# Optimization experiments

Measured on AMD Instinct MI355X. Metric: run time of the kernel, lower is better.

The kernel has to match this reference:

```python
import jax, jax.numpy as jnp
import numpy as np
from jax import lax

H = 64            # hidden size
NUM_LAYERS = 3
EMBED_LEN = 128
B, T = 256, 2048


def _lstm_layer(x, Wih, Whh, bih, bhh):
    """x: [B, T, in]; returns full hidden sequence [B, T, H].
    PyTorch gate order: i, f, g, o."""
    Bn = x.shape[0]
    b = bih + bhh  # [4H]
    # Precompute input contribution for all timesteps: [T, B, 4H]
    xg = jnp.einsum('bti,gi->tbg', x, Wih) + b
    h0 = jnp.zeros((Bn, H), x.dtype)
    c0 = jnp.zeros((Bn, H), x.dtype)

    def step(carry, xg_t):
        h, c = carry
        gates = xg_t + h @ Whh.T  # [B, 4H]
        i, f, g, o = jnp.split(gates, 4, axis=-1)
        i = jax.nn.sigmoid(i)
        f = jax.nn.sigmoid(f)
        g = jnp.tanh(g)
        o = jax.nn.sigmoid(o)
        c = f * c + i * g
        h = o * jnp.tanh(c)
        return (h, c), h

    (_, _), hs = lax.scan(step, (h0, c0), xg)  # hs: [T, B, H]
    return jnp.swapaxes(hs, 0, 1)              # [B, T, H]


def setup_inputs() -> dict:
    key = jax.random.key(0)
    ks = jax.random.split(key, 20)
    k = 1.0 / np.sqrt(H)  # PyTorch default init bound

    def u(kk, shape):
        return jax.random.uniform(kk, shape, jnp.float32, -k, k)

    inp = {"x": jax.random.normal(ks[0], (B, 1, T), jnp.float32)}
    in_sizes = [1, H, H]
    idx = 1
    for l in range(NUM_LAYERS):
        inp[f"Wih{l}"] = u(ks[idx], (4 * H, in_sizes[l])); idx += 1
        inp[f"Whh{l}"] = u(ks[idx], (4 * H, H)); idx += 1
        inp[f"bih{l}"] = u(ks[idx], (4 * H,)); idx += 1
        inp[f"bhh{l}"] = u(ks[idx], (4 * H,)); idx += 1
    inp["fcW"] = u(ks[idx], (EMBED_LEN, H)); idx += 1
    inp["fcb"] = u(ks[idx], (EMBED_LEN,))
    return inp


def reference(x, Wih0, Whh0, bih0, bhh0,
              Wih1, Whh1, bih1, bhh1,
              Wih2, Whh2, bih2, bhh2,
              fcW, fcb):
    # forward: transpose [B,1,T] -> [B,T,1]
    h = jnp.swapaxes(x, 1, 2)
    h = _lstm_layer(h, Wih0, Whh0, bih0, bhh0)
    h = _lstm_layer(h, Wih1, Whh1, bih1, bhh1)
    h = _lstm_layer(h, Wih2, Whh2, bih2, bhh2)
    last = h[:, -1, :]              # [B, H]
    return last @ fcW.T + fcb       # [B, EMBED_LEN]
```

## Files before the change

kernel.cpp:

```cpp
#include <hip/hip_runtime.h>

#define T_LEN 2048
#define HID 64
#define EMB 128
#define WD 8
#define NWIN (T_LEN / WD)
#define NPH (NWIN + 4)
#define PPAD (HID + 4)

typedef _Float16 half2_t __attribute__((ext_vector_type(2)));
typedef _Float16 half4 __attribute__((ext_vector_type(4)));
typedef _Float16 half8 __attribute__((ext_vector_type(8)));
typedef float f32x4 __attribute__((ext_vector_type(4)));
typedef unsigned uint4v __attribute__((ext_vector_type(4)));

#if __has_builtin(__builtin_amdgcn_exp2f)
#define EXP2F(x) __builtin_amdgcn_exp2f(x)
#else
#define EXP2F(x) exp2f(x)
#endif
#if __has_builtin(__builtin_amdgcn_rcpf)
#define RCPF(x) __builtin_amdgcn_rcpf(x)
#else
#define RCPF(x) (1.0f / (x))
#endif

#define LOG2E 1.4426950408889634f

__device__ __forceinline__ float fdot2(unsigned a, unsigned b, float c) {
    return __builtin_amdgcn_fdot2(__builtin_bit_cast(half2_t, a),
                                  __builtin_bit_cast(half2_t, b), c, false);
}

__device__ __forceinline__ float dotrow(const uint4v* w, const uint4v* g, float init) {
    float a0 = init, a1 = 0.f, a2 = 0.f, a3 = 0.f;
    #pragma unroll
    for (int q = 0; q < 8; ++q) {
        a0 = fdot2(w[q][0], g[q][0], a0);
        a1 = fdot2(w[q][1], g[q][1], a1);
        a2 = fdot2(w[q][2], g[q][2], a2);
        a3 = fdot2(w[q][3], g[q][3], a3);
    }
    return (a0 + a1) + (a2 + a3);
}

__device__ __forceinline__ uint4v pack8(float4 a, float4 b, float s) {
    half2_t h0{(_Float16)(a.x * s), (_Float16)(a.y * s)};
    half2_t h1{(_Float16)(a.z * s), (_Float16)(a.w * s)};
    half2_t h2{(_Float16)(b.x * s), (_Float16)(b.y * s)};
    half2_t h3{(_Float16)(b.z * s), (_Float16)(b.w * s)};
    uint4v q;
    q[0] = __builtin_bit_cast(unsigned, h0);
    q[1] = __builtin_bit_cast(unsigned, h1);
    q[2] = __builtin_bit_cast(unsigned, h2);
    q[3] = __builtin_bit_cast(unsigned, h3);
    return q;
}

__device__ __forceinline__ void cvt8(const float* __restrict__ Wp, float s, uint4v* dst) {
    const float4* p = reinterpret_cast<const float4*>(Wp);
    #pragma unroll
    for (int k = 0; k < 8; ++k) dst[k] = pack8(p[2 * k], p[2 * k + 1], s);
}

__global__ __launch_bounds__(512)
__attribute__((amdgpu_waves_per_eu(2, 2)))
void lstm3_fused(
    const float* __restrict__ x,
    const float* __restrict__ Wih0, const float* __restrict__ Whh0,
    const float* __restrict__ bih0, const float* __restrict__ bhh0,
    const float* __restrict__ Wih1, const float* __restrict__ Whh1,
    const float* __restrict__ bih1, const float* __restrict__ bhh1,
    const float* __restrict__ Wih2, const float* __restrict__ Whh2,
    const float* __restrict__ bih2, const float* __restrict__ bhh2,
    const float* __restrict__ fcW,  const float* __restrict__ fcb,
    float* __restrict__ out)
{
    const int b   = blockIdx.x;
    const int tid = threadIdx.x;
    const int wv  = tid >> 6;
    const int L   = tid & 63;

    __shared__ __align__(16) _Float16 h0ring[16][HID];
    __shared__ __align__(16) _Float16 h1ring[16][HID];
    __shared__ __align__(16) _Float16 h2ring[2][HID];
    __shared__ __align__(16) float p1buf[2][WD][4][PPAD];
    __shared__ __align__(16) float p2buf[2][WD][4][PPAD];
    __shared__ __align__(16) float xs[T_LEN];

    {
        const float4* xg4 = reinterpret_cast<const float4*>(x + b * T_LEN);
        reinterpret_cast<float4*>(xs)[tid] = xg4[tid];
        reinterpret_cast<unsigned*>(h0ring)[tid] = 0u;
        reinterpret_cast<unsigned*>(h1ring)[tid] = 0u;
        if (tid < 64) reinterpret_cast<unsigned*>(h2ring)[tid] = 0u;
    }

    const float sI = -LOG2E, sF = -LOG2E, sG = -2.f * LOG2E, sO = -LOG2E;
    const float scl[4] = {sI, sF, sG, sO};

    uint4v w[4][8];
    float bias4[4] = {0.f, 0.f, 0.f, 0.f};
    float wx4[4]   = {0.f, 0.f, 0.f, 0.f};

    if (wv < 3) {
        const float* Wh = (wv == 0) ? Whh0 : (wv == 1) ? Whh1 : Whh2;
        const float* bi = (wv == 0) ? bih0 : (wv == 1) ? bih1 : bih2;
        const float* bh = (wv == 0) ? bhh0 : (wv == 1) ? bhh1 : bhh2;
        #pragma unroll
        for (int c = 0; c < 4; ++c) {
            cvt8(Wh + (c * 64 + L) * 64, scl[c], w[c]);
            bias4[c] = (bi[c * 64 + L] + bh[c * 64 + L]) * scl[c];
        }
        if (wv == 0) {
            #pragma unroll
            for (int c = 0; c < 4; ++c) wx4[c] = Wih0[c * 64 + L] * scl[c];
        }
    } else if (wv == 3 || wv == 7) {
        const float* Wsrc = (wv == 3) ? Wih1 : Wih2;
        const int g4 = (L >> 4) * 4;
        const int mr = L & 15;
        #pragma unroll
        for (int t = 0; t < 16; ++t) {
            const float s = scl[t >> 2];
            const float* rowp = Wsrc + (t * 16 + mr) * 64;
            #pragma unroll
            for (int kf = 0; kf < 2; ++kf) {
                float4 lo = *reinterpret_cast<const float4*>(rowp + kf * 32 + g4);
                float4 hi = *reinterpret_cast<const float4*>(rowp + kf * 32 + 16 + g4);
                half8 a = {(_Float16)(lo.x * s), (_Float16)(lo.y * s),
                           (_Float16)(lo.z * s), (_Float16)(lo.w * s),
                           (_Float16)(hi.x * s), (_Float16)(hi.y * s),
                           (_Float16)(hi.z * s), (_Float16)(hi.w * s)};
                const int idx = t * 2 + kf;
                w[idx >> 3][idx & 7] = __builtin_bit_cast(uint4v, a);
            }
        }
    }

    float cst = 0.f;
    __syncthreads();

    for (int ph = 0; ph < NPH; ++ph) {
        const int par = ph & 1;

        if (wv == 0) {
            if (ph < NWIN) {
                _Float16* cur = &h0ring[par * 8][0];
                const _Float16* prv = &h0ring[(par ^ 1) * 8][0];
                const int tb = ph * WD;
                #pragma unroll
                for (int j = 0; j < WD; ++j) {
                    const uint4v* hp = reinterpret_cast<const uint4v*>(
                        (j == 0) ? (prv + 7 * HID) : (cur + (j - 1) * HID));
                    uint4v g[8];
                    #pragma unroll
                    for (int k = 0; k < 8; ++k) g[k] = hp[k];
                    float xv = xs[tb + j];
                    float d0 = dotrow(w[0], g, fmaf(wx4[0], xv, bias4[0]));
                    float d1 = dotrow(w[1], g, fmaf(wx4[1], xv, bias4[1]));
                    float d2 = dotrow(w[2], g, fmaf(wx4[2], xv, bias4[2]));
                    float d3 = dotrow(w[3], g, fmaf(wx4[3], xv, bias4[3]));
                    float ai = RCPF(1.f + EXP2F(d0));
                    float af = RCPF(1.f + EXP2F(d1));
                    float ag = fmaf(2.f, RCPF(1.f + EXP2F(d2)), -1.f);
                    float ao = RCPF(1.f + EXP2F(d3));
                    cst = fmaf(af, cst, ai * ag);
                    float tc = fmaf(2.f, RCPF(1.f + EXP2F(-2.f * LOG2E * cst)), -1.f);
                    cur[j * HID + L] = (_Float16)(ao * tc);
                }
            }
        } else if (wv == 1) {
            if (ph >= 2 && ph < NWIN + 2) {
                _Float16* cur = &h1ring[par * 8][0];
                const _Float16* prv = &h1ring[(par ^ 1) * 8][0];
                const float (*pb)[4][PPAD] = p1buf[par];
                #pragma unroll
                for (int j = 0; j < WD; ++j) {
                    const uint4v* hp = reinterpret_cast<const uint4v*>(
                        (j == 0) ? (prv + 7 * HID) : (cur + (j - 1) * HID));
                    uint4v g[8];
                    #pragma unroll
                    for (int k = 0; k < 8; ++k) g[k] = hp[k];
                    float d0 = dotrow(w[0], g, bias4[0] + pb[j][0][L]);
                    float d1 = dotrow(w[1], g, bias4[1] + pb[j][1][L]);
                    float d2 = dotrow(w[2], g, bias4[2] + pb[j][2][L]);
                    float d3 = dotrow(w[3], g, bias4[3] + pb[j][3][L]);
                    float ai = RCPF(1.f + EXP2F(d0));
                    float af = RCPF(1.f + EXP2F(d1));
                    float ag = fmaf(2.f, RCPF(1.f + EXP2F(d2)), -1.f);
                    float ao = RCPF(1.f + EXP2F(d3));
                    cst = fmaf(af, cst, ai * ag);
                    float tc = fmaf(2.f, RCPF(1.f + EXP2F(-2.f * LOG2E * cst)), -1.f);
                    cur[j * HID + L] = (_Float16)(ao * tc);
                }
            }
        } else if (wv == 2) {
            if (ph >= 4) {
                const float (*pb)[4][PPAD] = p2buf[par];
                #pragma unroll
                for (int j = 0; j < WD; ++j) {
                    const uint4v* hp = reinterpret_cast<const uint4v*>(
                        &h2ring[(j & 1) ^ 1][0]);
                    uint4v g[8];
                    #pragma unroll
                    for (int k = 0; k < 8; ++k) g[k] = hp[k];
                    float d0 = dotrow(w[0], g, bias4[0] + pb[j][0][L]);
                    float d1 = dotrow(w[1], g, bias4[1] + pb[j][1][L]);
                    float d2 = dotrow(w[2], g, bias4[2] + pb[j][2][L]);
                    float d3 = dotrow(w[3], g, bias4[3] + pb[j][3][L]);
                    float ai = RCPF(1.f + EXP2F(d0));
                    float af = RCPF(1.f + EXP2F(d1));
                    float ag = fmaf(2.f, RCPF(1.f + EXP2F(d2)), -1.f);
                    float ao = RCPF(1.f + EXP2F(d3));
                    cst = fmaf(af, cst, ai * ag);
                    float tc = fmaf(2.f, RCPF(1.f + EXP2F(-2.f * LOG2E * cst)), -1.f);
                    h2ring[j & 1][L] = (_Float16)(ao * tc);
                }
            }
        } else if (wv == 3 || wv == 7) {
            const bool act = (wv == 3) ? (ph >= 1 && ph < NWIN + 1)
                                       : (ph >= 3 && ph < NWIN + 3);
            if (act) {
                const _Float16 (*ring)[HID] = (wv == 3) ? h0ring : h1ring;
                float (*po)[4][PPAD] = ((wv == 3) ? p1buf : p2buf)[par ^ 1];
                const int jj = L & 7;
                const int g4 = (L >> 4) * 4;
                const _Float16* rb = &ring[(par ^ 1) * 8 + jj][0];
                half4 b00 = *reinterpret_cast<const half4*>(rb + g4);
                half4 b01 = *reinterpret_cast<const half4*>(rb + 16 + g4);
                half4 b10 = *reinterpret_cast<const half4*>(rb + 32 + g4);
                half4 b11 = *reinterpret_cast<const half4*>(rb + 48 + g4);
                half8 B0 = __builtin_shufflevector(b00, b01, 0, 1, 2, 3, 4, 5, 6, 7);
                half8 B1 = __builtin_shufflevector(b10, b11, 0, 1, 2, 3, 4, 5, 6, 7);
                f32x4 acc[16];
                #pragma unroll
                for (int t = 0; t < 16; ++t) {
                    const int i0 = t * 2, i1 = t * 2 + 1;
                    f32x4 z = {0.f, 0.f, 0.f, 0.f};
                    acc[t] = __builtin_amdgcn_mfma_f32_16x16x32_f16(
                        __builtin_bit_cast(half8, w[i0 >> 3][i0 & 7]), B0, z, 0, 0, 0);
                    acc[t] = __builtin_amdgcn_mfma_f32_16x16x32_f16(
                        __builtin_bit_cast(half8, w[i1 >> 3][i1 & 7]), B1, acc[t], 0, 0, 0);
                }
                if ((L & 15) < 8) {
                    #pragma unroll
                    for (int t = 0; t < 16; ++t) {
                        *reinterpret_cast<f32x4*>(
                            &po[jj][t >> 2][(t & 3) * 16 + g4]) = acc[t];
                    }
                }
            }
        }

        __syncthreads();
    }

    if (tid < EMB) {
        float acc = fcb[tid];
        const _Float16* hf = &h2ring[1][0];
        const float4* W4 = reinterpret_cast<const float4*>(fcW + tid * HID);
        #pragma unroll
        for (int k = 0; k < 16; ++k) {
            float4 wv4 = W4[k];
            acc = fmaf(wv4.x, (float)hf[4 * k + 0], acc);
            acc = fmaf(wv4.y, (float)hf[4 * k + 1], acc);
            acc = fmaf(wv4.z, (float)hf[4 * k + 2], acc);
            acc = fmaf(wv4.w, (float)hf[4 * k + 3], acc);
        }
        out[b * EMB + tid] = acc;
    }
}

extern "C" void kernel_launch(void* const* d_in, const int* in_sizes, int n_in,
                              void* d_out, int out_size, void* d_ws, size_t ws_size,
                              hipStream_t stream) {
    const float* x    = (const float*)d_in[0];
    const float* Wih0 = (const float*)d_in[1];
    const float* Whh0 = (const float*)d_in[2];
    const float* bih0 = (const float*)d_in[3];
    const float* bhh0 = (const float*)d_in[4];
    const float* Wih1 = (const float*)d_in[5];
    const float* Whh1 = (const float*)d_in[6];
    const float* bih1 = (const float*)d_in[7];
    const float* bhh1 = (const float*)d_in[8];
    const float* Wih2 = (const float*)d_in[9];
    const float* Whh2 = (const float*)d_in[10];
    const float* bih2 = (const float*)d_in[11];
    const float* bhh2 = (const float*)d_in[12];
    const float* fcW  = (const float*)d_in[13];
    const float* fcb  = (const float*)d_in[14];
    float* out = (float*)d_out;

    lstm3_fused<<<dim3(256), dim3(512), 0, stream>>>(
        x, Wih0, Whh0, bih0, bhh0,
        Wih1, Whh1, bih1, bhh1,
        Wih2, Whh2, bih2, bhh2,
        fcW, fcb, out);
}
```

Baseline: 1.021 ms.

## Process two batch sequences per block using all eight waves

Each block now handles two batch elements. Waves 0-2 and 4-6 each run the three recurrent layers for one sequence, and waves 3 and 7 run the layer-1 and layer-2 input-projection MFMAs for both sequences. The grid halves to 128 blocks, so the four previously idle waves do work and fewer blocks are launched on the 256-CU device. Ring buffer rows are padded to 72 halves, likely to reduce LDS bank conflicts. The trade-off is that the projection waves do twice the MFMA work per phase, which may lengthen the critical path of each phase.

```diff
diff --git a/kernel.cpp b/kernel.cpp
--- a/kernel.cpp
+++ b/kernel.cpp
@@ -7,6 +7,7 @@
 #define NWIN (T_LEN / WD)
 #define NPH (NWIN + 4)
 #define PPAD (HID + 4)
+#define RPAD 72
 
 typedef _Float16 half2_t __attribute__((ext_vector_type(2)));
 typedef _Float16 half4 __attribute__((ext_vector_type(4)));
@@ -76,24 +77,30 @@
     const float* __restrict__ fcW,  const float* __restrict__ fcb,
     float* __restrict__ out)
 {
-    const int b   = blockIdx.x;
-    const int tid = threadIdx.x;
-    const int wv  = tid >> 6;
-    const int L   = tid & 63;
-
-    __shared__ __align__(16) _Float16 h0ring[16][HID];
-    __shared__ __align__(16) _Float16 h1ring[16][HID];
-    __shared__ __align__(16) _Float16 h2ring[2][HID];
-    __shared__ __align__(16) float p1buf[2][WD][4][PPAD];
-    __shared__ __align__(16) float p2buf[2][WD][4][PPAD];
-    __shared__ __align__(16) float xs[T_LEN];
+    const int b    = blockIdx.x;
+    const int tid  = threadIdx.x;
+    const int wv   = tid >> 6;
+    const int role = wv & 3;
+    const int sp   = wv >> 2;
+    const int L    = tid & 63;
+
+    __shared__ __align__(16) _Float16 h0r[2][16][RPAD];
+    __shared__ __align__(16) _Float16 h1r[2][16][RPAD];
+    __shared__ __align__(16) _Float16 h2r[2][2][RPAD];
+    __shared__ __align__(16) float p1b[2][2][WD][4][PPAD];
+    __shared__ __align__(16) float p2b[2][2][WD][4][PPAD];
+    __shared__ __align__(16) float xs[2][T_LEN];
 
     {
-        const float4* xg4 = reinterpret_cast<const float4*>(x + b * T_LEN);
-        reinterpret_cast<float4*>(xs)[tid] = xg4[tid];
-        reinterpret_cast<unsigned*>(h0ring)[tid] = 0u;
-        reinterpret_cast<unsigned*>(h1ring)[tid] = 0u;
-        if (tid < 64) reinterpret_cast<unsigned*>(h2ring)[tid] = 0u;
+        const float4* xA = reinterpret_cast<const float4*>(x + (2 * b) * T_LEN);
+        const float4* xB = reinterpret_cast<const float4*>(x + (2 * b + 1) * T_LEN);
+        reinterpret_cast<float4*>(xs[0])[tid] = xA[tid];
+        reinterpret_cast<float4*>(xs[1])[tid] = xB[tid];
+        unsigned* z0 = reinterpret_cast<unsigned*>(h0r);
+        unsigned* z1 = reinterpret_cast<unsigned*>(h1r);
+        #pragma unroll
+        for (int i = tid; i < 1152; i += 512) { z0[i] = 0u; z1[i] = 0u; }
+        if (tid < 144) reinterpret_cast<unsigned*>(h2r)[tid] = 0u;
     }
 
     const float sI = -LOG2E, sF = -LOG2E, sG = -2.f * LOG2E, sO = -LOG2E;
@@ -103,21 +110,21 @@
     float bias4[4] = {0.f, 0.f, 0.f, 0.f};
     float wx4[4]   = {0.f, 0.f, 0.f, 0.f};
 
-    if (wv < 3) {
-        const float* Wh = (wv == 0) ? Whh0 : (wv == 1) ? Whh1 : Whh2;
-        const float* bi = (wv == 0) ? bih0 : (wv == 1) ? bih1 : bih2;
-        const float* bh = (wv == 0) ? bhh0 : (wv == 1) ? bhh1 : bhh2;
+    if (role < 3) {
+        const float* Wh = (role == 0) ? Whh0 : (role == 1) ? Whh1 : Whh2;
+        const float* bi = (role == 0) ? bih0 : (role == 1) ? bih1 : bih2;
+        const float* bh = (role == 0) ? bhh0 : (role == 1) ? bhh1 : bhh2;
         #pragma unroll
         for (int c = 0; c < 4; ++c) {
             cvt8(Wh + (c * 64 + L) * 64, scl[c], w[c]);
             bias4[c] = (bi[c * 64 + L] + bh[c * 64 + L]) * scl[c];
         }
-        if (wv == 0) {
+        if (role == 0) {
             #pragma unroll
             for (int c = 0; c < 4; ++c) wx4[c] = Wih0[c * 64 + L] * scl[c];
         }
-    } else if (wv == 3 || wv == 7) {
-        const float* Wsrc = (wv == 3) ? Wih1 : Wih2;
+    } else {
+        const float* Wsrc = (sp == 0) ? Wih1 : Wih2;
         const int g4 = (L >> 4) * 4;
         const int mr = L & 15;
         #pragma unroll
@@ -144,19 +151,19 @@
     for (int ph = 0; ph < NPH; ++ph) {
         const int par = ph & 1;
 
-        if (wv == 0) {
+        if (role == 0) {
             if (ph < NWIN) {
-                _Float16* cur = &h0ring[par * 8][0];
-                const _Float16* prv = &h0ring[(par ^ 1) * 8][0];
+                _Float16* cur = &h0r[sp][par * 8][0];
+                const _Float16* prv = &h0r[sp][(par ^ 1) * 8][0];
                 const int tb = ph * WD;
                 #pragma unroll
                 for (int j = 0; j < WD; ++j) {
                     const uint4v* hp = reinterpret_cast<const uint4v*>(
-                        (j == 0) ? (prv + 7 * HID) : (cur + (j - 1) * HID));
+                        (j == 0) ? (prv + 7 * RPAD) : (cur + (j - 1) * RPAD));
                     uint4v g[8];
                     #pragma unroll
                     for (int k = 0; k < 8; ++k) g[k] = hp[k];
-                    float xv = xs[tb + j];
+                    float xv = xs[sp][tb + j];
                     float d0 = dotrow(w[0], g, fmaf(wx4[0], xv, bias4[0]));
                     float d1 = dotrow(w[1], g, fmaf(wx4[1], xv, bias4[1]));
                     float d2 = dotrow(w[2], g, fmaf(wx4[2], xv, bias4[2]));
@@ -167,18 +174,18 @@
                     float ao = RCPF(1.f + EXP2F(d3));
                     cst = fmaf(af, cst, ai * ag);
                     float tc = fmaf(2.f, RCPF(1.f + EXP2F(-2.f * LOG2E * cst)), -1.f);
-                    cur[j * HID + L] = (_Float16)(ao * tc);
+                    cur[j * RPAD + L] = (_Float16)(ao * tc);
                 }
             }
-        } else if (wv == 1) {
+        } else if (role == 1) {
             if (ph >= 2 && ph < NWIN + 2) {
-                _Float16* cur = &h1ring[par * 8][0];
-                const _Float16* prv = &h1ring[(par ^ 1) * 8][0];
-                const float (*pb)[4][PPAD] = p1buf[par];
+                _Float16* cur = &h1r[sp][par * 8][0];
+                const _Float16* prv = &h1r[sp][(par ^ 1) * 8][0];
+                const float (*pb)[4][PPAD] = p1b[sp][par];
                 #pragma unroll
                 for (int j = 0; j < WD; ++j) {
                     const uint4v* hp = reinterpret_cast<const uint4v*>(
-                        (j == 0) ? (prv + 7 * HID) : (cur + (j - 1) * HID));
+                        (j == 0) ? (prv + 7 * RPAD) : (cur + (j - 1) * RPAD));
                     uint4v g[8];
                     #pragma unroll
                     for (int k = 0; k < 8; ++k) g[k] = hp[k];
@@ -192,16 +199,16 @@
                     float ao = RCPF(1.f + EXP2F(d3));
                     cst = fmaf(af, cst, ai * ag);
                     float tc = fmaf(2.f, RCPF(1.f + EXP2F(-2.f * LOG2E * cst)), -1.f);
-                    cur[j * HID + L] = (_Float16)(ao * tc);
+                    cur[j * RPAD + L] = (_Float16)(ao * tc);
                 }
             }
-        } else if (wv == 2) {
+        } else if (role == 2) {
             if (ph >= 4) {
-                const float (*pb)[4][PPAD] = p2buf[par];
+                const float (*pb)[4][PPAD] = p2b[sp][par];
                 #pragma unroll
                 for (int j = 0; j < WD; ++j) {
                     const uint4v* hp = reinterpret_cast<const uint4v*>(
-                        &h2ring[(j & 1) ^ 1][0]);
+                        &h2r[sp][(j & 1) ^ 1][0]);
                     uint4v g[8];
                     #pragma unroll
                     for (int k = 0; k < 8; ++k) g[k] = hp[k];
@@ -215,39 +222,41 @@
                     float ao = RCPF(1.f + EXP2F(d3));
                     cst = fmaf(af, cst, ai * ag);
                     float tc = fmaf(2.f, RCPF(1.f + EXP2F(-2.f * LOG2E * cst)), -1.f);
-                    h2ring[j & 1][L] = (_Float16)(ao * tc);
+                    h2r[sp][j & 1][L] = (_Float16)(ao * tc);
                 }
             }
-        } else if (wv == 3 || wv == 7) {
-            const bool act = (wv == 3) ? (ph >= 1 && ph < NWIN + 1)
+        } else {
+            const bool act = (sp == 0) ? (ph >= 1 && ph < NWIN + 1)
                                        : (ph >= 3 && ph < NWIN + 3);
             if (act) {
-                const _Float16 (*ring)[HID] = (wv == 3) ? h0ring : h1ring;
-                float (*po)[4][PPAD] = ((wv == 3) ? p1buf : p2buf)[par ^ 1];
                 const int jj = L & 7;
                 const int g4 = (L >> 4) * 4;
-                const _Float16* rb = &ring[(par ^ 1) * 8 + jj][0];
-                half4 b00 = *reinterpret_cast<const half4*>(rb + g4);
-                half4 b01 = *reinterpret_cast<const half4*>(rb + 16 + g4);
-                half4 b10 = *reinterpret_cast<const half4*>(rb + 32 + g4);
-                half4 b11 = *reinterpret_cast<const half4*>(rb + 48 + g4);
-                half8 B0 = __builtin_shufflevector(b00, b01, 0, 1, 2, 3, 4, 5, 6, 7);
-                half8 B1 = __builtin_shufflevector(b10, b11, 0, 1, 2, 3, 4, 5, 6, 7);
-                f32x4 acc[16];
+                const bool storeOK = (L & 15) < 8;
                 #pragma unroll
-                for (int t = 0; t < 16; ++t) {
-                    const int i0 = t * 2, i1 = t * 2 + 1;
-                    f32x4 z = {0.f, 0.f, 0.f, 0.f};
-                    acc[t] = __builtin_amdgcn_mfma_f32_16x16x32_f16(
-                        __builtin_bit_cast(half8, w[i0 >> 3][i0 & 7]), B0, z, 0, 0, 0);
-                    acc[t] = __builtin_amdgcn_mfma_f32_16x16x32_f16(
-                        __builtin_bit_cast(half8, w[i1 >> 3][i1 & 7]), B1, acc[t], 0, 0, 0);
-                }
-                if ((L & 15) < 8) {
+                for (int ss = 0; ss < 2; ++ss) {
+                    const _Float16 (*ring)[RPAD] =
+                        (sp == 0) ? h0r[ss] : h1r[ss];
+                    float* poJJ = (sp == 0)
+                        ? &p1b[ss][par ^ 1][jj][0][0]
+                        : &p2b[ss][par ^ 1][jj][0][0];
+                    const _Float16* rb = &ring[(par ^ 1) * 8 + jj][0];
+                    half4 b00 = *reinterpret_cast<const half4*>(rb + g4);
+                    half4 b01 = *reinterpret_cast<const half4*>(rb + 16 + g4);
+                    half4 b10 = *reinterpret_cast<const half4*>(rb + 32 + g4);
+                    half4 b11 = *reinterpret_cast<const half4*>(rb + 48 + g4);
+                    half8 B0 = __builtin_shufflevector(b00, b01, 0, 1, 2, 3, 4, 5, 6, 7);
+                    half8 B1 = __builtin_shufflevector(b10, b11, 0, 1, 2, 3, 4, 5, 6, 7);
                     #pragma unroll
                     for (int t = 0; t < 16; ++t) {
-                        *reinterpret_cast<f32x4*>(
-                            &po[jj][t >> 2][(t & 3) * 16 + g4]) = acc[t];
+                        const int i0 = t * 2, i1 = t * 2 + 1;
+                        f32x4 z = {0.f, 0.f, 0.f, 0.f};
+                        f32x4 a = __builtin_amdgcn_mfma_f32_16x16x32_f16(
+                            __builtin_bit_cast(half8, w[i0 >> 3][i0 & 7]), B0, z, 0, 0, 0);
+                        a = __builtin_amdgcn_mfma_f32_16x16x32_f16(
+                            __builtin_bit_cast(half8, w[i1 >> 3][i1 & 7]), B1, a, 0, 0, 0);
+                        if (storeOK)
+                            *reinterpret_cast<f32x4*>(
+                                poJJ + (t >> 2) * PPAD + (t & 3) * 16 + g4) = a;
                     }
                 }
             }
@@ -256,10 +265,12 @@
         __syncthreads();
     }
 
-    if (tid < EMB) {
-        float acc = fcb[tid];
-        const _Float16* hf = &h2ring[1][0];
-        const float4* W4 = reinterpret_cast<const float4*>(fcW + tid * HID);
+    if (tid < 2 * EMB) {
+        const int s = tid >> 7;
+        const int r = tid & 127;
+        float acc = fcb[r];
+        const _Float16* hf = &h2r[s][1][0];
+        const float4* W4 = reinterpret_cast<const float4*>(fcW + r * HID);
         #pragma unroll
         for (int k = 0; k < 16; ++k) {
             float4 wv4 = W4[k];
@@ -268,7 +279,7 @@
             acc = fmaf(wv4.z, (float)hf[4 * k + 2], acc);
             acc = fmaf(wv4.w, (float)hf[4 * k + 3], acc);
         }
-        out[b * EMB + tid] = acc;
+        out[(2 * b + s) * EMB + r] = acc;
     }
 }
 
@@ -292,7 +303,7 @@
     const float* fcb  = (const float*)d_in[14];
     float* out = (float*)d_out;
 
-    lstm3_fused<<<dim3(256), dim3(512), 0, stream>>>(
+    lstm3_fused<<<dim3(128), dim3(512), 0, stream>>>(
         x, Wih0, Whh0, bih0, bhh0,
         Wih1, Whh1, bih1, bhh1,
         Wih2, Whh2, bih2, bhh2,
```

Result: slower. 1.578 ms (+54.5%).

## Split each LSTM layer across two waves with K-split and per-step barriers

Applied to the files above, without the earlier changes.

Each layer's recurrence now runs on two waves, each owning 32 hidden units, with lanes splitting the 64-long dot product into halves combined via cross-lane shuffle. The input-projection MFMA waves move to waves 6 and 7 and are interleaved across the timesteps of each window. Synchronization moves from one barrier per 8-step window to one per timestep, and the hidden rings are padded and enlarged to 16 slots for all layers. This shortens the serial per-step dot chain at the cost of many more block barriers and shuffle latency.

```diff
diff --git a/kernel.cpp b/kernel.cpp
--- a/kernel.cpp
+++ b/kernel.cpp
@@ -6,11 +6,12 @@
 #define WD 8
 #define NWIN (T_LEN / WD)
 #define NPH (NWIN + 4)
-#define PPAD (HID + 4)
+#define PPAD 68
+#define RPAD 72
 
 typedef _Float16 half2_t __attribute__((ext_vector_type(2)));
-typedef _Float16 half4 __attribute__((ext_vector_type(4)));
-typedef _Float16 half8 __attribute__((ext_vector_type(8)));
+typedef _Float16 half4v __attribute__((ext_vector_type(4)));
+typedef _Float16 half8v __attribute__((ext_vector_type(8)));
 typedef float f32x4 __attribute__((ext_vector_type(4)));
 typedef unsigned uint4v __attribute__((ext_vector_type(4)));
 
@@ -32,14 +33,14 @@
                                   __builtin_bit_cast(half2_t, b), c, false);
 }
 
-__device__ __forceinline__ float dotrow(const uint4v* w, const uint4v* g, float init) {
+__device__ __forceinline__ float dot32(const uint4v* w4, const uint4v* g, float init) {
     float a0 = init, a1 = 0.f, a2 = 0.f, a3 = 0.f;
     #pragma unroll
-    for (int q = 0; q < 8; ++q) {
-        a0 = fdot2(w[q][0], g[q][0], a0);
-        a1 = fdot2(w[q][1], g[q][1], a1);
-        a2 = fdot2(w[q][2], g[q][2], a2);
-        a3 = fdot2(w[q][3], g[q][3], a3);
+    for (int q = 0; q < 4; ++q) {
+        a0 = fdot2(w4[q][0], g[q][0], a0);
+        a1 = fdot2(w4[q][1], g[q][1], a1);
+        a2 = fdot2(w4[q][2], g[q][2], a2);
+        a3 = fdot2(w4[q][3], g[q][3], a3);
     }
     return (a0 + a1) + (a2 + a3);
 }
@@ -57,15 +58,9 @@
     return q;
 }
 
-__device__ __forceinline__ void cvt8(const float* __restrict__ Wp, float s, uint4v* dst) {
-    const float4* p = reinterpret_cast<const float4*>(Wp);
-    #pragma unroll
-    for (int k = 0; k < 8; ++k) dst[k] = pack8(p[2 * k], p[2 * k + 1], s);
-}
-
 __global__ __launch_bounds__(512)
 __attribute__((amdgpu_waves_per_eu(2, 2)))
-void lstm3_fused(
+void lstm3_split(
     const float* __restrict__ x,
     const float* __restrict__ Wih0, const float* __restrict__ Whh0,
     const float* __restrict__ bih0, const float* __restrict__ bhh0,
@@ -81,19 +76,30 @@
     const int wv  = tid >> 6;
     const int L   = tid & 63;
 
-    __shared__ __align__(16) _Float16 h0ring[16][HID];
-    __shared__ __align__(16) _Float16 h1ring[16][HID];
-    __shared__ __align__(16) _Float16 h2ring[2][HID];
-    __shared__ __align__(16) float p1buf[2][WD][4][PPAD];
-    __shared__ __align__(16) float p2buf[2][WD][4][PPAD];
+    const bool isC = (wv < 6);
+    const int lay  = wv >> 1;
+    const int e    = 32 * (wv & 1) + (L & 31);
+    const int kb   = (L >> 5) * 32;
+    const bool kh0 = (L < 32);
+    const int g4p  = (L >> 4) * 4;
+    const int mr   = L & 15;
+    const int jj   = L & 7;
+
+    __shared__ __align__(16) _Float16 h0r[16][RPAD];
+    __shared__ __align__(16) _Float16 h1r[16][RPAD];
+    __shared__ __align__(16) _Float16 h2r[16][RPAD];
+    __shared__ __align__(16) float p1b[2][WD][4][PPAD];
+    __shared__ __align__(16) float p2b[2][WD][4][PPAD];
     __shared__ __align__(16) float xs[T_LEN];
 
     {
         const float4* xg4 = reinterpret_cast<const float4*>(x + b * T_LEN);
         reinterpret_cast<float4*>(xs)[tid] = xg4[tid];
-        reinterpret_cast<unsigned*>(h0ring)[tid] = 0u;
-        reinterpret_cast<unsigned*>(h1ring)[tid] = 0u;
-        if (tid < 64) reinterpret_cast<unsigned*>(h2ring)[tid] = 0u;
+        for (int i = tid; i < 576; i += 512) {
+            reinterpret_cast<unsigned*>(h0r)[i] = 0u;
+            reinterpret_cast<unsigned*>(h1r)[i] = 0u;
+            reinterpret_cast<unsigned*>(h2r)[i] = 0u;
+        }
     }
 
     const float sI = -LOG2E, sF = -LOG2E, sG = -2.f * LOG2E, sO = -LOG2E;
@@ -103,170 +109,142 @@
     float bias4[4] = {0.f, 0.f, 0.f, 0.f};
     float wx4[4]   = {0.f, 0.f, 0.f, 0.f};
 
-    if (wv < 3) {
-        const float* Wh = (wv == 0) ? Whh0 : (wv == 1) ? Whh1 : Whh2;
-        const float* bi = (wv == 0) ? bih0 : (wv == 1) ? bih1 : bih2;
-        const float* bh = (wv == 0) ? bhh0 : (wv == 1) ? bhh1 : bhh2;
+    if (isC) {
+        const float* Wh = (lay == 0) ? Whh0 : (lay == 1) ? Whh1 : Whh2;
+        const float* bi = (lay == 0) ? bih0 : (lay == 1) ? bih1 : bih2;
+        const float* bh = (lay == 0) ? bhh0 : (lay == 1) ? bhh1 : bhh2;
         #pragma unroll
         for (int c = 0; c < 4; ++c) {
-            cvt8(Wh + (c * 64 + L) * 64, scl[c], w[c]);
-            bias4[c] = (bi[c * 64 + L] + bh[c * 64 + L]) * scl[c];
-        }
-        if (wv == 0) {
+            const float4* p = reinterpret_cast<const float4*>(Wh + (c * 64 + e) * 64 + kb);
+            w[c][0] = pack8(p[0], p[1], scl[c]);
+            w[c][1] = pack8(p[2], p[3], scl[c]);
+            w[c][2] = pack8(p[4], p[5], scl[c]);
+            w[c][3] = pack8(p[6], p[7], scl[c]);
+            bias4[c] = (bi[c * 64 + e] + bh[c * 64 + e]) * scl[c];
+        }
+        if (lay == 0) {
             #pragma unroll
-            for (int c = 0; c < 4; ++c) wx4[c] = Wih0[c * 64 + L] * scl[c];
-        }
-    } else if (wv == 3 || wv == 7) {
-        const float* Wsrc = (wv == 3) ? Wih1 : Wih2;
-        const int g4 = (L >> 4) * 4;
-        const int mr = L & 15;
-        #pragma unroll
-        for (int t = 0; t < 16; ++t) {
-            const float s = scl[t >> 2];
-            const float* rowp = Wsrc + (t * 16 + mr) * 64;
+            for (int c = 0; c < 4; ++c) wx4[c] = Wih0[c * 64 + e] * scl[c];
+        }
+    } else {
+        const float* Wsrc = (wv == 6) ? Wih1 : Wih2;
+        #pragma unroll
+        for (int tt = 0; tt < 16; ++tt) {
+            const float s = scl[tt >> 2];
+            const float* rowp = Wsrc + (tt * 16 + mr) * 64;
             #pragma unroll
             for (int kf = 0; kf < 2; ++kf) {
-                float4 lo = *reinterpret_cast<const float4*>(rowp + kf * 32 + g4);
-                float4 hi = *reinterpret_cast<const float4*>(rowp + kf * 32 + 16 + g4);
-                half8 a = {(_Float16)(lo.x * s), (_Float16)(lo.y * s),
-                           (_Float16)(lo.z * s), (_Float16)(lo.w * s),
-                           (_Float16)(hi.x * s), (_Float16)(hi.y * s),
-                           (_Float16)(hi.z * s), (_Float16)(hi.w * s)};
-                const int idx = t * 2 + kf;
+                float4 lo = *reinterpret_cast<const float4*>(rowp + kf * 32 + g4p);
+                float4 hi = *reinterpret_cast<const float4*>(rowp + kf * 32 + 16 + g4p);
+                half8v a = {(_Float16)(lo.x * s), (_Float16)(lo.y * s),
+                            (_Float16)(lo.z * s), (_Float16)(lo.w * s),
+                            (_Float16)(hi.x * s), (_Float16)(hi.y * s),
+                            (_Float16)(hi.z * s), (_Float16)(hi.w * s)};
+                const int idx = tt * 2 + kf;
                 w[idx >> 3][idx & 7] = __builtin_bit_cast(uint4v, a);
             }
         }
     }
 
-    float cst = 0.f;
+    _Float16 (*ring)[RPAD] = (lay == 0) ? h0r : (lay == 1) ? h1r : h2r;
+    const float* pbase = (lay == 1) ? &p1b[0][0][0][0] : &p2b[0][0][0][0];
+    _Float16 (*pring)[RPAD] = (wv == 6) ? h0r : h1r;
+    float* pobase = (wv == 6) ? &p1b[0][0][0][0] : &p2b[0][0][0][0];
+
+    float cs = 0.f;
     __syncthreads();
 
     for (int ph = 0; ph < NPH; ++ph) {
         const int par = ph & 1;
-
-        if (wv == 0) {
-            if (ph < NWIN) {
-                _Float16* cur = &h0ring[par * 8][0];
-                const _Float16* prv = &h0ring[(par ^ 1) * 8][0];
-                const int tb = ph * WD;
-                #pragma unroll
-                for (int j = 0; j < WD; ++j) {
+        half8v B0{}, B1{};
+        bool act;
+        int tbase = 0;
+        float* po = nullptr;
+        const float* pb = nullptr;
+
+        if (isC) {
+            act = (ph >= 2 * lay) && (ph < NWIN + 2 * lay);
+            tbase = (ph - 2 * lay) * WD;
+            pb = pbase + par * (WD * 4 * PPAD);
+        } else {
+            const int pp = (wv - 6) * 2;
+            act = (ph >= 1 + pp) && (ph <= NWIN + pp);
+            if (act) {
+                const _Float16* rb = &pring[(par ^ 1) * 8 + jj][0];
+                half4v b00 = *reinterpret_cast<const half4v*>(rb + g4p);
+                half4v b01 = *reinterpret_cast<const half4v*>(rb + 16 + g4p);
+                half4v b10 = *reinterpret_cast<const half4v*>(rb + 32 + g4p);
+                half4v b11 = *reinterpret_cast<const half4v*>(rb + 48 + g4p);
+                B0 = __builtin_shufflevector(b00, b01, 0, 1, 2, 3, 4, 5, 6, 7);
+                B1 = __builtin_shufflevector(b10, b11, 0, 1, 2, 3, 4, 5, 6, 7);
+                po = pobase + (par ^ 1) * (WD * 4 * PPAD);
+            }
+        }
+
+        #pragma unroll
+        for (int j = 0; j < WD; ++j) {
+            if (isC) {
+                if (act) {
+                    const int t = tbase + j;
                     const uint4v* hp = reinterpret_cast<const uint4v*>(
-                        (j == 0) ? (prv + 7 * HID) : (cur + (j - 1) * HID));
-                    uint4v g[8];
-                    #pragma unroll
-                    for (int k = 0; k < 8; ++k) g[k] = hp[k];
-                    float xv = xs[tb + j];
-                    float d0 = dotrow(w[0], g, fmaf(wx4[0], xv, bias4[0]));
-                    float d1 = dotrow(w[1], g, fmaf(wx4[1], xv, bias4[1]));
-                    float d2 = dotrow(w[2], g, fmaf(wx4[2], xv, bias4[2]));
-                    float d3 = dotrow(w[3], g, fmaf(wx4[3], xv, bias4[3]));
+                        &ring[(t - 1) & 15][kb]);
+                    uint4v g[4] = {hp[0], hp[1], hp[2], hp[3]};
+                    float ext[4];
+                    if (lay == 0) {
+                        const float xv = xs[t];
+                        #pragma unroll
+                        for (int c = 0; c < 4; ++c) ext[c] = fmaf(wx4[c], xv, bias4[c]);
+                    } else {
+                        #pragma unroll
+                        for (int c = 0; c < 4; ++c)
+                            ext[c] = bias4[c] + pb[(j * 4 + c) * PPAD + e];
+                    }
+                    float d0 = dot32(w[0], g, kh0 ? ext[0] : 0.f);
+                    float d1 = dot32(w[1], g, kh0 ? ext[1] : 0.f);
+                    float d2 = dot32(w[2], g, kh0 ? ext[2] : 0.f);
+                    float d3 = dot32(w[3], g, kh0 ? ext[3] : 0.f);
+                    d0 += __shfl_xor(d0, 32, 64);
+                    d1 += __shfl_xor(d1, 32, 64);
+                    d2 += __shfl_xor(d2, 32, 64);
+                    d3 += __shfl_xor(d3, 32, 64);
                     float ai = RCPF(1.f + EXP2F(d0));
                     float af = RCPF(1.f + EXP2F(d1));
                     float ag = fmaf(2.f, RCPF(1.f + EXP2F(d2)), -1.f);
                     float ao = RCPF(1.f + EXP2F(d3));
-                    cst = fmaf(af, cst, ai * ag);
-                    float tc = fmaf(2.f, RCPF(1.f + EXP2F(-2.f * LOG2E * cst)), -1.f);
-                    cur[j * HID + L] = (_Float16)(ao * tc);
+                    cs = fmaf(af, cs, ai * ag);
+                    float tc = fmaf(2.f, RCPF(1.f + EXP2F(-2.f * LOG2E * cs)), -1.f);
+                    if (kh0) ring[t & 15][e] = (_Float16)(ao * tc);
+                }
+            } else if (act) {
+                #pragma unroll
+                for (int u = 0; u < 2; ++u) {
+                    const int tt = 2 * j + u;
+                    const int i0 = 2 * tt, i1 = 2 * tt + 1;
+                    f32x4 z = {0.f, 0.f, 0.f, 0.f};
+                    f32x4 a = __builtin_amdgcn_mfma_f32_16x16x32_f16(
+                        __builtin_bit_cast(half8v, w[i0 >> 3][i0 & 7]), B0, z, 0, 0, 0);
+                    a = __builtin_amdgcn_mfma_f32_16x16x32_f16(
+                        __builtin_bit_cast(half8v, w[i1 >> 3][i1 & 7]), B1, a, 0, 0, 0);
+                    if (mr < 8)
+                        *reinterpret_cast<f32x4*>(
+                            po + (jj * 4 + (tt >> 2)) * PPAD + (tt & 3) * 16 + g4p) = a;
                 }
             }
-        } else if (wv == 1) {
-            if (ph >= 2 && ph < NWIN + 2) {
-                _Float16* cur = &h1ring[par * 8][0];
-                const _Float16* prv = &h1ring[(par ^ 1) * 8][0];
-                const float (*pb)[4][PPAD] = p1buf[par];
-                #pragma unroll
-                for (int j = 0; j < WD; ++j) {
-                    const uint4v* hp = reinterpret_cast<const uint4v*>(
-                        (j == 0) ? (prv + 7 * HID) : (cur + (j - 1) * HID));
-                    uint4v g[8];
-                    #pragma unroll
-                    for (int k = 0; k < 8; ++k) g[k] = hp[k];
-                    float d0 = dotrow(w[0], g, bias4[0] + pb[j][0][L]);
-                    float d1 = dotrow(w[1], g, bias4[1] + pb[j][1][L]);
-                    float d2 = dotrow(w[2], g, bias4[2] + pb[j][2][L]);
-                    float d3 = dotrow(w[3], g, bias4[3] + pb[j][3][L]);
-                    float ai = RCPF(1.f + EXP2F(d0));
-                    float af = RCPF(1.f + EXP2F(d1));
-                    float ag = fmaf(2.f, RCPF(1.f + EXP2F(d2)), -1.f);
-                    float ao = RCPF(1.f + EXP2F(d3));
-                    cst = fmaf(af, cst, ai * ag);
-                    float tc = fmaf(2.f, RCPF(1.f + EXP2F(-2.f * LOG2E * cst)), -1.f);
-                    cur[j * HID + L] = (_Float16)(ao * tc);
-                }
-            }
-        } else if (wv == 2) {
-            if (ph >= 4) {
-                const float (*pb)[4][PPAD] = p2buf[par];
-                #pragma unroll
-                for (int j = 0; j < WD; ++j) {
-                    const uint4v* hp = reinterpret_cast<const uint4v*>(
-                        &h2ring[(j & 1) ^ 1][0]);
-                    uint4v g[8];
-                    #pragma unroll
-                    for (int k = 0; k < 8; ++k) g[k] = hp[k];
-                    float d0 = dotrow(w[0], g, bias4[0] + pb[j][0][L]);
-                    float d1 = dotrow(w[1], g, bias4[1] + pb[j][1][L]);
-                    float d2 = dotrow(w[2], g, bias4[2] + pb[j][2][L]);
-                    float d3 = dotrow(w[3], g, bias4[3] + pb[j][3][L]);
-                    float ai = RCPF(1.f + EXP2F(d0));
-                    float af = RCPF(1.f + EXP2F(d1));
-                    float ag = fmaf(2.f, RCPF(1.f + EXP2F(d2)), -1.f);
-                    float ao = RCPF(1.f + EXP2F(d3));
-                    cst = fmaf(af, cst, ai * ag);
-                    float tc = fmaf(2.f, RCPF(1.f + EXP2F(-2.f * LOG2E * cst)), -1.f);
-                    h2ring[j & 1][L] = (_Float16)(ao * tc);
-                }
-            }
-        } else if (wv == 3 || wv == 7) {
-            const bool act = (wv == 3) ? (ph >= 1 && ph < NWIN + 1)
-                                       : (ph >= 3 && ph < NWIN + 3);
-            if (act) {
-                const _Float16 (*ring)[HID] = (wv == 3) ? h0ring : h1ring;
-                float (*po)[4][PPAD] = ((wv == 3) ? p1buf : p2buf)[par ^ 1];
-                const int jj = L & 7;
-                const int g4 = (L >> 4) * 4;
-                const _Float16* rb = &ring[(par ^ 1) * 8 + jj][0];
-                half4 b00 = *reinterpret_cast<const half4*>(rb + g4);
-                half4 b01 = *reinterpret_cast<const half4*>(rb + 16 + g4);
-                half4 b10 = *reinterpret_cast<const half4*>(rb + 32 + g4);
-                half4 b11 = *reinterpret_cast<const half4*>(rb + 48 + g4);
-                half8 B0 = __builtin_shufflevector(b00, b01, 0, 1, 2, 3, 4, 5, 6, 7);
-                half8 B1 = __builtin_shufflevector(b10, b11, 0, 1, 2, 3, 4, 5, 6, 7);
-                f32x4 acc[16];
-                #pragma unroll
-                for (int t = 0; t < 16; ++t) {
-                    const int i0 = t * 2, i1 = t * 2 + 1;
-                    f32x4 z = {0.f, 0.f, 0.f, 0.f};
-                    acc[t] = __builtin_amdgcn_mfma_f32_16x16x32_f16(
-                        __builtin_bit_cast(half8, w[i0 >> 3][i0 & 7]), B0, z, 0, 0, 0);
-                    acc[t] = __builtin_amdgcn_mfma_f32_16x16x32_f16(
-                        __builtin_bit_cast(half8, w[i1 >> 3][i1 & 7]), B1, acc[t], 0, 0, 0);
-                }
-                if ((L & 15) < 8) {
-                    #pragma unroll
-                    for (int t = 0; t < 16; ++t) {
-                        *reinterpret_cast<f32x4*>(
-                            &po[jj][t >> 2][(t & 3) * 16 + g4]) = acc[t];
-                    }
-                }
-            }
-        }
-
-        __syncthreads();
+            __syncthreads();
+        }
     }
 
     if (tid < EMB) {
         float acc = fcb[tid];
-        const _Float16* hf = &h2ring[1][0];
+        const _Float16* hf2 = &h2r[15][0];
         const float4* W4 = reinterpret_cast<const float4*>(fcW + tid * HID);
         #pragma unroll
         for (int k = 0; k < 16; ++k) {
-            float4 wv4 = W4[k];
-            acc = fmaf(wv4.x, (float)hf[4 * k + 0], acc);
-            acc = fmaf(wv4.y, (float)hf[4 * k + 1], acc);
-            acc = fmaf(wv4.z, (float)hf[4 * k + 2], acc);
-            acc = fmaf(wv4.w, (float)hf[4 * k + 3], acc);
+            float4 w4 = W4[k];
+            acc = fmaf(w4.x, (float)hf2[4 * k + 0], acc);
+            acc = fmaf(w4.y, (float)hf2[4 * k + 1], acc);
+            acc = fmaf(w4.z, (float)hf2[4 * k + 2], acc);
+            acc = fmaf(w4.w, (float)hf2[4 * k + 3], acc);
         }
         out[b * EMB + tid] = acc;
     }
@@ -292,7 +270,7 @@
     const float* fcb  = (const float*)d_in[14];
     float* out = (float*)d_out;
 
-    lstm3_fused<<<dim3(256), dim3(512), 0, stream>>>(
+    lstm3_split<<<dim3(256), dim3(512), 0, stream>>>(
         x, Wih0, Whh0, bih0, bhh0,
         Wih1, Whh1, bih1, bhh1,
         Wih2, Whh2, bih2, bhh2,
```

New measurement: 1.592 ms. 1.56x slower.
